# Kernel tuning notes

Hardware: AMD Instinct MI355X
Metric: run time of the kernel (lower is better)

Reference implementation:

```python
import jax, jax.numpy as jnp
import numpy as np

D = 1024   # d_model
HS = 64    # head_size
H = D // HS
B, T = 4, 2048
EPS = 1e-5


def setup_inputs() -> dict:
    key = jax.random.key(0)
    ks = jax.random.split(key, 8)
    s = 1.0 / np.sqrt(D)
    mk = lambda k: (jax.random.normal(k, (D, D), jnp.float32) * s)
    return {
        "x": jax.random.normal(ks[0], (B, T, D), jnp.float32),
        "ln_g": jnp.ones((D,), jnp.float32),
        "ln_b": jnp.zeros((D,), jnp.float32),
        "Wx": mk(ks[1]),
        "Ww": mk(ks[2]),
        "bw": jnp.zeros((D,), jnp.float32),
        "Wk": mk(ks[3]),
        "Wv": mk(ks[4]),
        "Wr": mk(ks[5]),
        "Wo": mk(ks[6]),
    }


def reference(x, ln_g, ln_b, Wx, Ww, bw, Wk, Wv, Wr, Wo):
    Bb, Tt, C = x.shape
    nh, hs = C // HS, HS
    # LayerNorm (population variance, matching torch nn.LayerNorm)
    mu = x.mean(-1, keepdims=True)
    var = x.var(-1, keepdims=True)
    xn = (x - mu) / jnp.sqrt(var + EPS) * ln_g + ln_b
    # projections (weights stored pre-transposed: y = x @ W)
    w = jax.nn.sigmoid((xn @ Wx) @ Ww + bw).reshape(Bb, Tt, nh, hs)
    k = (xn @ Wk).reshape(Bb, Tt, nh, hs)
    v = (xn @ Wv).reshape(Bb, Tt, nh, hs)
    r = jax.nn.sigmoid(xn @ Wr).reshape(Bb, Tt, nh, hs)

    def step(state, inp):
        kt, vt, wt, rt = inp  # each [B, H, hs]
        # outer product kv [B,H,hs,hs]; row-wise decay by (1 - w_t)
        state = (1.0 - wt)[..., None] * state + kt[..., None] * vt[..., None, :]
        out = jnp.einsum('bhd,bhde->bhe', rt, state)
        return state, out

    init = jnp.zeros((Bb, nh, hs, hs), x.dtype)
    tm = lambda a: jnp.moveaxis(a, 1, 0)  # time-major for scan
    state, outs = jax.lax.scan(step, init, (tm(k), tm(v), tm(w), tm(r)))
    y = jnp.moveaxis(outs, 0, 1).reshape(Bb, Tt, C) @ Wo
    return (y, state)
```

## Files before the change

### kernel.cpp

```cpp
#include <hip/hip_runtime.h>

#define ROWS 8192
#define DD   1024
#define TT   2048
#define NH   16
#define HS   64
#define CH   32
#define NC   (TT / CH)

typedef __attribute__((ext_vector_type(8))) short short8;
typedef __attribute__((ext_vector_type(4))) float f32x4;
typedef __attribute__((ext_vector_type(4))) unsigned short us4;
typedef unsigned short u16;

__device__ __forceinline__ u16 f2bf(float f) {
  unsigned u = __builtin_bit_cast(unsigned, f);
  u += 0x7fffu + ((u >> 16) & 1u);
  return (u16)(u >> 16);
}

__device__ __forceinline__ float bf2f(u16 h) {
  return __builtin_bit_cast(float, (unsigned)h << 16);
}

__device__ __forceinline__ void gload16(const void* g, void* l) {
  __builtin_amdgcn_global_load_lds(
      (const __attribute__((address_space(1))) unsigned int*)g,
      (__attribute__((address_space(3))) unsigned int*)l, 16, 0, 0);
}

__global__ __launch_bounds__(256) void transpose_cast(const float* __restrict__ W,
                                                      u16* __restrict__ WT) {
  __shared__ float tile[32][33];
  const int tx = threadIdx.x, ty = threadIdx.y;
  const int bx = blockIdx.x, by = blockIdx.y;
#pragma unroll
  for (int j = 0; j < 4; ++j)
    tile[ty + j * 8][tx] = W[(size_t)(by * 32 + ty + j * 8) * DD + bx * 32 + tx];
  __syncthreads();
#pragma unroll
  for (int j = 0; j < 4; ++j)
    WT[(size_t)(bx * 32 + ty + j * 8) * DD + by * 32 + tx] = f2bf(tile[tx][ty + j * 8]);
}

__global__ __launch_bounds__(256) void ln_kernel(const float* __restrict__ x,
                                                 const float* __restrict__ g,
                                                 const float* __restrict__ b,
                                                 u16* __restrict__ xn) {
  const int row = blockIdx.x;
  const int tid = threadIdx.x;
  const float4 v = reinterpret_cast<const float4*>(x + (size_t)row * DD)[tid];
  float s = v.x + v.y + v.z + v.w;
  float s2 = v.x * v.x + v.y * v.y + v.z * v.z + v.w * v.w;
#pragma unroll
  for (int o = 32; o > 0; o >>= 1) { s += __shfl_down(s, o); s2 += __shfl_down(s2, o); }
  __shared__ float red[8];
  const int wv = tid >> 6;
  if ((tid & 63) == 0) { red[wv] = s; red[4 + wv] = s2; }
  __syncthreads();
  s = red[0] + red[1] + red[2] + red[3];
  s2 = red[4] + red[5] + red[6] + red[7];
  const float mu = s * (1.f / 1024.f);
  const float var = s2 * (1.f / 1024.f) - mu * mu;
  const float rstd = rsqrtf(var + 1e-5f);
  const float4 gg = reinterpret_cast<const float4*>(g)[tid];
  const float4 bb = reinterpret_cast<const float4*>(b)[tid];
  us4 o4;
  o4.x = f2bf((v.x - mu) * rstd * gg.x + bb.x);
  o4.y = f2bf((v.y - mu) * rstd * gg.y + bb.y);
  o4.z = f2bf((v.z - mu) * rstd * gg.z + bb.z);
  o4.w = f2bf((v.w - mu) * rstd * gg.w + bb.w);
  *reinterpret_cast<us4*>(xn + (size_t)row * DD + tid * 4) = o4;
}

template <int EPI>
__global__ __launch_bounds__(256) void gemm_bt(const u16* __restrict__ A,
                                               const u16* __restrict__ BT,
                                               float* __restrict__ Cf,
                                               u16* __restrict__ Cb,
                                               const float* __restrict__ bias,
                                               int M, int N, int K) {
  __shared__ u16 lA[2][128 * 32];
  __shared__ u16 lB[2][128 * 32];
  const int tid = threadIdx.x;
  const int bx = blockIdx.x, by = blockIdx.y;
  const int lane = tid & 63, wid = tid >> 6;
  const int wr = wid >> 1, wc = wid & 1;
  const int sr = tid >> 2, sc = (tid & 3) * 8;
  const u16* gA = A + (size_t)(by * 128 + sr) * K + sc;
  const u16* gB = BT + (size_t)(bx * 128 + sr) * K + sc;

  f32x4 acc[4][4];
#pragma unroll
  for (int m = 0; m < 4; ++m)
#pragma unroll
    for (int n = 0; n < 4; ++n) acc[m][n] = (f32x4){0.f, 0.f, 0.f, 0.f};

  auto stage = [&](int buf, int kt) {
    const u16* a0 = gA + kt * 32;
    const u16* b0 = gB + kt * 32;
    gload16(a0, &lA[buf][tid * 8]);
    gload16(a0 + (size_t)64 * K, &lA[buf][2048 + tid * 8]);
    gload16(b0, &lB[buf][tid * 8]);
    gload16(b0 + (size_t)64 * K, &lB[buf][2048 + tid * 8]);
  };

  stage(0, 0);
  const int fr = lane & 15, fk = (lane >> 4) * 8;
  int cur = 0;
  const int nk = K / 32;
  for (int kt = 0; kt < nk; ++kt) {
    __syncthreads();
    if (kt + 1 < nk) stage(cur ^ 1, kt + 1);
    short8 af[4], bv[4];
#pragma unroll
    for (int m = 0; m < 4; ++m)
      af[m] = *reinterpret_cast<const short8*>(&lA[cur][(wr * 64 + m * 16 + fr) * 32 + fk]);
#pragma unroll
    for (int n = 0; n < 4; ++n)
      bv[n] = *reinterpret_cast<const short8*>(&lB[cur][(wc * 64 + n * 16 + fr) * 32 + fk]);
#pragma unroll
    for (int m = 0; m < 4; ++m)
#pragma unroll
      for (int n = 0; n < 4; ++n)
        acc[m][n] = __builtin_amdgcn_mfma_f32_16x16x32_bf16(af[m], bv[n], acc[m][n], 0, 0, 0);
    cur ^= 1;
  }

  const int er = (lane >> 4) * 4, ec = lane & 15;
#pragma unroll
  for (int m = 0; m < 4; ++m) {
    const int row0 = by * 128 + wr * 64 + m * 16 + er;
#pragma unroll
    for (int n = 0; n < 4; ++n) {
      const int col = bx * 128 + wc * 64 + n * 16 + ec;
#pragma unroll
      for (int i = 0; i < 4; ++i) {
        const float val = acc[m][n][i];
        const size_t idx = (size_t)(row0 + i) * N + col;
        if constexpr (EPI == 0) {
          Cb[idx] = f2bf(val);
        } else if constexpr (EPI == 1) {
          Cf[idx] = val;
        } else if constexpr (EPI == 2) {
          Cf[idx] = 1.f / (1.f + __expf(-val));
        } else {
          const float z = val + bias[col];
          Cf[idx] = 1.f / (1.f + __expf(z));
        }
      }
    }
  }
}

__global__ __launch_bounds__(256) void scan_phase1(const float* __restrict__ omw,
                                                   const float* __restrict__ kk,
                                                   const float* __restrict__ vv,
                                                   u16* __restrict__ U,
                                                   float* __restrict__ P) {
  const int c = blockIdx.x, bh = blockIdx.y;
  const int tid = threadIdx.x;
  const int lane = tid & 63;
  const int dbase = __builtin_amdgcn_readfirstlane((tid >> 6) << 4);
  const size_t chainBase = (size_t)(bh >> 4) * TT * DD + (size_t)(bh & 15) * HS;
  size_t base = chainBase + (size_t)c * CH * DD;

  float st[16];
#pragma unroll
  for (int i = 0; i < 16; ++i) st[i] = 0.f;
  const int pd = dbase + (lane & 15);
  float vp = 1.f;

  float ve = vv[base + lane];
  for (int t = 0; t < CH; ++t) {
    const float* __restrict__ op = omw + base;
    const float* __restrict__ kp = kk + base;
    const size_t nbase = (t + 1 < CH) ? (base + DD) : base;
    const float ve_n = vv[nbase + lane];
    vp *= op[pd];
#pragma unroll
    for (int i = 0; i < 16; ++i)
      st[i] = __builtin_fmaf(op[dbase + i], st[i], kp[dbase + i] * ve);
    ve = ve_n;
    base += DD;
  }
  u16* __restrict__ Ub = U + ((size_t)c * 64 + bh) * 4096;
#pragma unroll
  for (int i = 0; i < 16; ++i) Ub[(dbase + i) * 64 + lane] = f2bf(st[i]);
  if (lane < 16) P[((size_t)c * 64 + bh) * 64 + dbase + lane] = vp;
}

__global__ __launch_bounds__(256) void scan_phase2(u16* __restrict__ U,
                                                   const float* __restrict__ P,
                                                   float* __restrict__ stateOut) {
  const int bh = blockIdx.x;
  const int ds = blockIdx.y;
  const int tid = threadIdx.x;
  const int d = ds * 4 + (tid >> 6);
  const int e = tid & 63;
  const size_t el = (size_t)d * 64 + e;

  float S = 0.f;
  size_t ub = (size_t)bh * 4096 + el;
  size_t pb = (size_t)bh * 64 + d;
  u16 u_c = U[ub];
  float p_c = P[pb];
  for (int c = 0; c < NC; ++c) {
    u16 u_n = u_c; float p_n = p_c;
    if (c + 1 < NC) {
      u_n = U[ub + (size_t)64 * 4096];
      p_n = P[pb + (size_t)64 * 64];
    }
    U[ub] = f2bf(S);
    S = __builtin_fmaf(p_c, S, bf2f(u_c));
    u_c = u_n; p_c = p_n;
    ub += (size_t)64 * 4096;
    pb += (size_t)64 * 64;
  }
  stateOut[(size_t)bh * 4096 + el] = S;
}

__global__ __launch_bounds__(256) void scan_phase3(const float* __restrict__ omw,
                                                   const float* __restrict__ kk,
                                                   const float* __restrict__ vv,
                                                   const float* __restrict__ rr,
                                                   const u16* __restrict__ S_start,
                                                   u16* __restrict__ outs) {
  __shared__ float part[4][16][64];
  const int c = blockIdx.x, bh = blockIdx.y;
  const int tid = threadIdx.x;
  const int lane = tid & 63;
  const int wid = tid >> 6;
  const int dbase = __builtin_amdgcn_readfirstlane(wid << 4);
  const size_t chainBase = (size_t)(bh >> 4) * TT * DD + (size_t)(bh & 15) * HS;
  const size_t base0 = chainBase + (size_t)c * CH * DD;
  size_t base = base0;

  float st[16];
  const u16* __restrict__ Sb = S_start + ((size_t)c * 64 + bh) * 4096;
#pragma unroll
  for (int i = 0; i < 16; ++i) st[i] = bf2f(Sb[(dbase + i) * 64 + lane]);

  float ve = vv[base + lane];
  for (int w2 = 0; w2 < CH / 16; ++w2) {
#pragma unroll
    for (int tt = 0; tt < 16; ++tt) {
      const float* __restrict__ op = omw + base;
      const float* __restrict__ kp = kk + base;
      const float* __restrict__ rp = rr + base;
      const size_t nbase = (w2 * 16 + tt + 1 < CH) ? (base + DD) : base;
      const float ve_n = vv[nbase + lane];

      float a0 = 0.f, a1 = 0.f;
#pragma unroll
      for (int i = 0; i < 8; ++i) {
        st[i] = __builtin_fmaf(op[dbase + i], st[i], kp[dbase + i] * ve);
        a0 = __builtin_fmaf(rp[dbase + i], st[i], a0);
        st[8 + i] = __builtin_fmaf(op[dbase + 8 + i], st[8 + i], kp[dbase + 8 + i] * ve);
        a1 = __builtin_fmaf(rp[dbase + 8 + i], st[8 + i], a1);
      }
      part[wid][tt][lane] = a0 + a1;
      ve = ve_n;
      base += DD;
    }
    __syncthreads();
#pragma unroll
    for (int s = 0; s < 4; ++s) {
      const int tt = wid * 4 + s;
      const float sum = (part[0][tt][lane] + part[1][tt][lane]) +
                        (part[2][tt][lane] + part[3][tt][lane]);
      outs[base0 + (size_t)(w2 * 16 + tt) * DD + lane] = f2bf(sum);
    }
    __syncthreads();
  }
}

extern "C" void kernel_launch(void* const* d_in, const int* in_sizes, int n_in,
                              void* d_out, int out_size, void* d_ws, size_t ws_size,
                              hipStream_t stream) {
  const float* x   = (const float*)d_in[0];
  const float* lng = (const float*)d_in[1];
  const float* lnb = (const float*)d_in[2];
  const float* Wx  = (const float*)d_in[3];
  const float* Ww  = (const float*)d_in[4];
  const float* bw  = (const float*)d_in[5];
  const float* Wk  = (const float*)d_in[6];
  const float* Wv  = (const float*)d_in[7];
  const float* Wr  = (const float*)d_in[8];
  const float* Wo  = (const float*)d_in[9];
  float* out = (float*)d_out;
  char* ws = (char*)d_ws;

  const size_t SZ_W = (size_t)DD * DD * 2;
  u16* WxT = (u16*)(ws + 0 * SZ_W);
  u16* WwT = (u16*)(ws + 1 * SZ_W);
  u16* WkT = (u16*)(ws + 2 * SZ_W);
  u16* WvT = (u16*)(ws + 3 * SZ_W);
  u16* WrT = (u16*)(ws + 4 * SZ_W);
  u16* WoT = (u16*)(ws + 5 * SZ_W);
  size_t off = 6 * SZ_W;
  const size_t SZ_ABF = (size_t)ROWS * DD * 2;
  u16* xn   = (u16*)(ws + off); off += SZ_ABF;
  u16* pbuf = (u16*)(ws + off); off += SZ_ABF;
  u16* outs = (u16*)(ws + off); off += SZ_ABF;
  const size_t SZ_AF = (size_t)ROWS * DD * 4;
  float* omw = (float*)(ws + off); off += SZ_AF;
  float* kf  = (float*)(ws + off); off += SZ_AF;
  float* vf  = (float*)(ws + off); off += SZ_AF;
  float* rf  = (float*)(ws + off); off += SZ_AF;
  u16*   Ubuf = xn;
  float* Pbuf = (float*)WxT;
  (void)ws_size; (void)in_sizes; (void)n_in; (void)out_size;

  dim3 tpb(32, 8), tgrid(32, 32);
  transpose_cast<<<tgrid, tpb, 0, stream>>>(Wx, WxT);
  transpose_cast<<<tgrid, tpb, 0, stream>>>(Ww, WwT);
  transpose_cast<<<tgrid, tpb, 0, stream>>>(Wk, WkT);
  transpose_cast<<<tgrid, tpb, 0, stream>>>(Wv, WvT);
  transpose_cast<<<tgrid, tpb, 0, stream>>>(Wr, WrT);
  transpose_cast<<<tgrid, tpb, 0, stream>>>(Wo, WoT);

  ln_kernel<<<ROWS, 256, 0, stream>>>(x, lng, lnb, xn);

  dim3 ggrid(DD / 128, ROWS / 128), gblk(256);
  gemm_bt<0><<<ggrid, gblk, 0, stream>>>(xn, WxT, nullptr, pbuf, nullptr, ROWS, DD, DD);
  gemm_bt<3><<<ggrid, gblk, 0, stream>>>(pbuf, WwT, omw, nullptr, bw, ROWS, DD, DD);
  gemm_bt<1><<<ggrid, gblk, 0, stream>>>(xn, WkT, kf, nullptr, nullptr, ROWS, DD, DD);
  gemm_bt<1><<<ggrid, gblk, 0, stream>>>(xn, WvT, vf, nullptr, nullptr, ROWS, DD, DD);
  gemm_bt<2><<<ggrid, gblk, 0, stream>>>(xn, WrT, rf, nullptr, nullptr, ROWS, DD, DD);

  dim3 sgrid(NC, 64);
  scan_phase1<<<sgrid, 256, 0, stream>>>(omw, kf, vf, Ubuf, Pbuf);
  dim3 p2grid(64, 16);
  scan_phase2<<<p2grid, 256, 0, stream>>>(Ubuf, Pbuf, out + (size_t)ROWS * DD);
  scan_phase3<<<sgrid, 256, 0, stream>>>(omw, kf, vf, rf, Ubuf, outs);

  gemm_bt<1><<<ggrid, gblk, 0, stream>>>(outs, WoT, out, nullptr, nullptr, ROWS, DD, DD);
}
```

Before: 495.8 us.

## Stage scan inputs through double-buffered LDS windows in chunked scan phases

Scan phases 1 and 3 now copy 16-timestep windows of decay, k, v (and r) into double-buffered shared memory with gload16 async-style copies. The next window is prefetched while the current one is consumed. The inner loops then read float4 vectors from LDS instead of issuing scalar global loads per timestep. This targets load latency in the sequential recurrence, at the cost of extra LDS use and block syncs, which may lower occupancy.

```diff
diff --git a/kernel.cpp b/kernel.cpp
--- a/kernel.cpp
+++ b/kernel.cpp
@@ -158,12 +158,25 @@
                                                    const float* __restrict__ vv,
                                                    u16* __restrict__ U,
                                                    float* __restrict__ P) {
+  __shared__ float win[2 * 3072];
   const int c = blockIdx.x, bh = blockIdx.y;
   const int tid = threadIdx.x;
   const int lane = tid & 63;
-  const int dbase = __builtin_amdgcn_readfirstlane((tid >> 6) << 4);
+  const int wid = tid >> 6;
+  const int dbase = __builtin_amdgcn_readfirstlane(wid << 4);
   const size_t chainBase = (size_t)(bh >> 4) * TT * DD + (size_t)(bh & 15) * HS;
-  size_t base = chainBase + (size_t)c * CH * DD;
+  const size_t base0 = chainBase + (size_t)c * CH * DD;
+
+  auto stage = [&](int buf, int w2) {
+#pragma unroll
+    for (int j = 0; j < 3; ++j) {
+      const int idx = tid + 256 * j;
+      const int a = idx >> 8, rem = idx & 255, tt = rem >> 4, f4c = rem & 15;
+      const float* s = (a == 0) ? omw : (a == 1) ? kk : vv;
+      gload16(s + base0 + (size_t)(w2 * 16 + tt) * DD + f4c * 4,
+              &win[buf * 3072 + idx * 4]);
+    }
+  };
 
   float st[16];
 #pragma unroll
@@ -171,18 +184,29 @@
   const int pd = dbase + (lane & 15);
   float vp = 1.f;
 
-  float ve = vv[base + lane];
-  for (int t = 0; t < CH; ++t) {
-    const float* __restrict__ op = omw + base;
-    const float* __restrict__ kp = kk + base;
-    const size_t nbase = (t + 1 < CH) ? (base + DD) : base;
-    const float ve_n = vv[nbase + lane];
-    vp *= op[pd];
-#pragma unroll
-    for (int i = 0; i < 16; ++i)
-      st[i] = __builtin_fmaf(op[dbase + i], st[i], kp[dbase + i] * ve);
-    ve = ve_n;
-    base += DD;
+  stage(0, 0);
+  __syncthreads();
+  int buf = 0;
+  for (int w2 = 0; w2 < CH / 16; ++w2) {
+    if (w2 + 1 < CH / 16) stage(buf ^ 1, w2 + 1);
+    const float* wb = &win[buf * 3072];
+#pragma unroll
+    for (int tt = 0; tt < 16; ++tt) {
+      const float4* o4 = (const float4*)&wb[       tt * 64 + dbase];
+      const float4* k4 = (const float4*)&wb[1024 + tt * 64 + dbase];
+      const float ve  = wb[2048 + tt * 64 + lane];
+      vp *= wb[tt * 64 + pd];
+#pragma unroll
+      for (int i4 = 0; i4 < 4; ++i4) {
+        const float4 o = o4[i4], k = k4[i4];
+        st[4*i4+0] = __builtin_fmaf(o.x, st[4*i4+0], k.x * ve);
+        st[4*i4+1] = __builtin_fmaf(o.y, st[4*i4+1], k.y * ve);
+        st[4*i4+2] = __builtin_fmaf(o.z, st[4*i4+2], k.z * ve);
+        st[4*i4+3] = __builtin_fmaf(o.w, st[4*i4+3], k.w * ve);
+      }
+    }
+    __syncthreads();
+    buf ^= 1;
   }
   u16* __restrict__ Ub = U + ((size_t)c * 64 + bh) * 4096;
 #pragma unroll
@@ -226,6 +250,7 @@
                                                    const float* __restrict__ rr,
                                                    const u16* __restrict__ S_start,
                                                    u16* __restrict__ outs) {
+  __shared__ float win[2 * 4096];
   __shared__ float part[4][16][64];
   const int c = blockIdx.x, bh = blockIdx.y;
   const int tid = threadIdx.x;
@@ -234,34 +259,49 @@
   const int dbase = __builtin_amdgcn_readfirstlane(wid << 4);
   const size_t chainBase = (size_t)(bh >> 4) * TT * DD + (size_t)(bh & 15) * HS;
   const size_t base0 = chainBase + (size_t)c * CH * DD;
-  size_t base = base0;
+
+  auto stage = [&](int buf, int w2) {
+#pragma unroll
+    for (int j = 0; j < 4; ++j) {
+      const int idx = tid + 256 * j;
+      const int a = idx >> 8, rem = idx & 255, tt = rem >> 4, f4c = rem & 15;
+      const float* s = (a == 0) ? omw : (a == 1) ? kk : (a == 2) ? rr : vv;
+      gload16(s + base0 + (size_t)(w2 * 16 + tt) * DD + f4c * 4,
+              &win[buf * 4096 + idx * 4]);
+    }
+  };
 
   float st[16];
   const u16* __restrict__ Sb = S_start + ((size_t)c * 64 + bh) * 4096;
 #pragma unroll
   for (int i = 0; i < 16; ++i) st[i] = bf2f(Sb[(dbase + i) * 64 + lane]);
 
-  float ve = vv[base + lane];
+  stage(0, 0);
+  __syncthreads();
+  int buf = 0;
   for (int w2 = 0; w2 < CH / 16; ++w2) {
+    if (w2 + 1 < CH / 16) stage(buf ^ 1, w2 + 1);
+    const float* wb = &win[buf * 4096];
 #pragma unroll
     for (int tt = 0; tt < 16; ++tt) {
-      const float* __restrict__ op = omw + base;
-      const float* __restrict__ kp = kk + base;
-      const float* __restrict__ rp = rr + base;
-      const size_t nbase = (w2 * 16 + tt + 1 < CH) ? (base + DD) : base;
-      const float ve_n = vv[nbase + lane];
-
+      const float4* o4 = (const float4*)&wb[       tt * 64 + dbase];
+      const float4* k4 = (const float4*)&wb[1024 + tt * 64 + dbase];
+      const float4* r4 = (const float4*)&wb[2048 + tt * 64 + dbase];
+      const float ve  = wb[3072 + tt * 64 + lane];
       float a0 = 0.f, a1 = 0.f;
 #pragma unroll
-      for (int i = 0; i < 8; ++i) {
-        st[i] = __builtin_fmaf(op[dbase + i], st[i], kp[dbase + i] * ve);
-        a0 = __builtin_fmaf(rp[dbase + i], st[i], a0);
-        st[8 + i] = __builtin_fmaf(op[dbase + 8 + i], st[8 + i], kp[dbase + 8 + i] * ve);
-        a1 = __builtin_fmaf(rp[dbase + 8 + i], st[8 + i], a1);
+      for (int i4 = 0; i4 < 4; ++i4) {
+        const float4 o = o4[i4], k = k4[i4], r = r4[i4];
+        st[4*i4+0] = __builtin_fmaf(o.x, st[4*i4+0], k.x * ve);
+        a0 = __builtin_fmaf(r.x, st[4*i4+0], a0);
+        st[4*i4+1] = __builtin_fmaf(o.y, st[4*i4+1], k.y * ve);
+        a1 = __builtin_fmaf(r.y, st[4*i4+1], a1);
+        st[4*i4+2] = __builtin_fmaf(o.z, st[4*i4+2], k.z * ve);
+        a0 = __builtin_fmaf(r.z, st[4*i4+2], a0);
+        st[4*i4+3] = __builtin_fmaf(o.w, st[4*i4+3], k.w * ve);
+        a1 = __builtin_fmaf(r.w, st[4*i4+3], a1);
       }
       part[wid][tt][lane] = a0 + a1;
-      ve = ve_n;
-      base += DD;
     }
     __syncthreads();
 #pragma unroll
@@ -272,6 +312,7 @@
       outs[base0 + (size_t)(w2 * 16 + tt) * DD + lane] = f2bf(sum);
     }
     __syncthreads();
+    buf ^= 1;
   }
 }
 
```

After: 473.2 us. -4.5%, faster.
